# Kernel optimization log

Measured on AMD Instinct MI355X. Metric: run time of the kernel, lower is better.

## Reference

```python
import jax, jax.numpy as jnp
import numpy as np

B, S, H = 2, 2048, 2048
NH, NKV, HD = 16, 4, 128
GROUPS = NH // NKV
THETA = 10000.0
EPS = 1e-6


def setup_inputs() -> dict:
    key = jax.random.key(0)
    ks = jax.random.split(key, 6)
    scale = 0.02
    return {
        "hidden_states": jax.random.normal(ks[0], (B, S, H), jnp.float32),
        "wq": jax.random.normal(ks[1], (NH * HD, H), jnp.float32) * scale,
        "wk": jax.random.normal(ks[2], (NKV * HD, H), jnp.float32) * scale,
        "wv": jax.random.normal(ks[3], (NKV * HD, H), jnp.float32) * scale,
        "wo": jax.random.normal(ks[4], (H, NH * HD), jnp.float32) * scale,
        "q_norm_weight": jnp.ones((HD,), jnp.float32),
        "k_norm_weight": jnp.ones((HD,), jnp.float32),
    }


def _rope_tables(seq_len):
    inv_freq = 1.0 / (THETA ** (jnp.arange(0, HD, 2, dtype=jnp.float32) / HD))
    t = jnp.arange(seq_len, dtype=jnp.float32)
    freqs = jnp.outer(t, inv_freq)              # [S, HD/2]
    emb = jnp.concatenate([freqs, freqs], -1)   # [S, HD]
    return jnp.cos(emb), jnp.sin(emb)


def _rotate_half(x):
    x1, x2 = x[..., : HD // 2], x[..., HD // 2:]
    return jnp.concatenate([-x2, x1], -1)


def _rmsnorm(x, w):
    var = jnp.mean(jnp.square(x), axis=-1, keepdims=True)
    return x * jax.lax.rsqrt(var + EPS) * w


def reference(hidden_states, wq, wk, wv, wo, q_norm_weight, k_norm_weight):
    b, s, _ = hidden_states.shape
    q = (hidden_states @ wq.T).reshape(b, s, NH, HD).transpose(0, 2, 1, 3)    # [b,nh,s,d]
    k = (hidden_states @ wk.T).reshape(b, s, NKV, HD).transpose(0, 2, 1, 3)   # [b,nkv,s,d]
    v = (hidden_states @ wv.T).reshape(b, s, NKV, HD).transpose(0, 2, 1, 3)

    cos, sin = _rope_tables(s)                  # [s,d]
    q = q * cos + _rotate_half(q) * sin
    k = k * cos + _rotate_half(k) * sin

    # fused QK RMSNorm (applied inside fused_qknorm_flash_attention)
    q = _rmsnorm(q, q_norm_weight)
    k = _rmsnorm(k, k_norm_weight)

    # GQA: share each kv head across GROUPS query heads without materializing repeats
    qg = q.reshape(b, NKV, GROUPS, s, HD)
    scale = 1.0 / jnp.sqrt(jnp.float32(HD))
    scores = jnp.einsum('bhgqd,bhkd->bhgqk', qg, k) * scale   # [b,nkv,g,s,s]
    causal = jnp.tril(jnp.ones((s, s), bool))
    scores = jnp.where(causal, scores, jnp.finfo(scores.dtype).min)
    probs = jax.nn.softmax(scores, axis=-1)
    out = jnp.einsum('bhgqk,bhkd->bhgqd', probs, v)            # [b,nkv,g,s,d]
    out = out.reshape(b, NH, s, HD).transpose(0, 2, 1, 3).reshape(b, s, NH * HD)
    return out @ wo.T
```

## Files before the change

kernel.cpp:

```cpp
#include <hip/hip_runtime.h>
#include <math.h>

typedef __bf16 bf16;
typedef __bf16 bf16x8 __attribute__((ext_vector_type(8)));
typedef __bf16 bf16x4 __attribute__((ext_vector_type(4)));
typedef float f32x4 __attribute__((ext_vector_type(4)));

#define B_DIM 2
#define S_LEN 2048
#define H_DIM 2048
#define NH 16
#define NKV 4
#define HD 128

__device__ __forceinline__ void gl_lds16(const void* g, void* l) {
    __builtin_amdgcn_global_load_lds(
        (const __attribute__((address_space(1))) unsigned int*)g,
        (__attribute__((address_space(3))) unsigned int*)l, 16, 0, 0);
}

__device__ __forceinline__ void bar() {
    asm volatile("" ::: "memory");
    __builtin_amdgcn_s_barrier();
    asm volatile("" ::: "memory");
}

__global__ __launch_bounds__(256) void cast_all(const float* __restrict__ s0,
                                                const float* __restrict__ s1,
                                                const float* __restrict__ s2,
                                                const float* __restrict__ s3,
                                                const float* __restrict__ s4,
                                                bf16* __restrict__ dst) {
    const int i = blockIdx.x * 256 + threadIdx.x;
    const float* src;
    int off;
    if (i < 2097152)      { src = s0; off = 0; }
    else if (i < 3145728) { src = s1; off = 2097152; }
    else if (i < 3407872) { src = s2; off = 3145728; }
    else if (i < 3670016) { src = s3; off = 3407872; }
    else                  { src = s4; off = 3670016; }
    float4 f = ((const float4*)src)[i - off];
    bf16x4 o = { (bf16)f.x, (bf16)f.y, (bf16)f.z, (bf16)f.w };
    *(bf16x4*)(dst + (size_t)i * 4) = o;
}

template <typename OutT>
__global__ __launch_bounds__(512, 2) void gemm256(const bf16* __restrict__ A,
                                                  const bf16* __restrict__ Bt,
                                                  OutT* __restrict__ C,
                                                  int M, int N, int K) {
    __shared__ __align__(16) bf16 smem[65536];
    const int t = threadIdx.x, lane = t & 63, w = t >> 6;
    const int lr = lane & 15, quad = lane >> 4;
    const int nN = N >> 8;
    const int nwg = gridDim.x, chunk = nwg >> 3;
    const int bid = blockIdx.x;
    const int lid = (bid & 7) * chunk + (bid >> 3);
    const int m0 = (lid / nN) << 8, n0 = (lid % nN) << 8;
    const int mh_w = w >> 2;
    const int wn = (w & 3) << 6;
    const int nh_w = (w & 3) >> 1;
    const int rb = (w & 1) << 6;
    const int nK = K >> 6;
    const int nIter = K >> 7;

    const int ld0 = w * 2;
    const int lrow = lane >> 2;
    const int csrc = (lane & 3) ^ ((lane >> 3) & 3);
    const int swz = (lr >> 1) & 3;

    auto stA = [&](int ts, int mh) {
        if (ts < nK) {
            bf16* db = smem + (ts & 1) * 16384 + mh * 8192;
            const bf16* sp = A + (size_t)(m0 + mh * 128) * K + ts * 64;
#pragma unroll
            for (int i = 0; i < 2; i++) {
                const int ldi = ld0 + i, kb = ldi >> 3, rg = ldi & 7;
                gl_lds16(sp + (size_t)(rg * 16 + lrow) * K + kb * 32 + csrc * 8,
                         db + kb * 4096 + rg * 512);
            }
        }
    };
    auto stB = [&](int ts, int nh) {
        if (ts < nK) {
            bf16* db = smem + 32768 + (ts & 1) * 16384 + nh * 8192;
            const bf16* sp = Bt + (size_t)(n0 + nh * 128) * K + ts * 64;
#pragma unroll
            for (int i = 0; i < 2; i++) {
                const int ldi = ld0 + i, kb = ldi >> 3, rg = ldi & 7;
                gl_lds16(sp + (size_t)(rg * 16 + lrow) * K + kb * 32 + csrc * 8,
                         db + kb * 4096 + rg * 512);
            }
        }
    };

    f32x4 acc[8][4];
#pragma unroll
    for (int i = 0; i < 8; i++)
#pragma unroll
        for (int j = 0; j < 4; j++) acc[i][j] = (f32x4){0.f, 0.f, 0.f, 0.f};
    bf16x8 af[8], b0[4], b1[4];

    auto rdA = [&](int s, int fi0) {
        const bf16* bp = smem + s * 16384 + mh_w * 8192;
#pragma unroll
        for (int f = 0; f < 4; f++)
#pragma unroll
            for (int ks = 0; ks < 2; ks++)
                af[f * 2 + ks] = *(const bf16x8*)(bp + ks * 4096 +
                                                  ((fi0 + f) * 16 + lr) * 32 + (quad ^ swz) * 8);
    };
    auto rdB = [&](int s, int fj0, bf16x8* dst) {
        const bf16* bp = smem + 32768 + s * 16384 + nh_w * 8192;
#pragma unroll
        for (int f = 0; f < 2; f++)
#pragma unroll
            for (int ks = 0; ks < 2; ks++)
                dst[f * 2 + ks] = *(const bf16x8*)(bp + ks * 4096 +
                                                   (rb + (fj0 + f) * 16 + lr) * 32 + (quad ^ swz) * 8);
    };
    auto mm16 = [&](int fi0, int fj0, bf16x8* bb) {
        __builtin_amdgcn_s_setprio(1);
#pragma unroll
        for (int f = 0; f < 4; f++)
#pragma unroll
            for (int g = 0; g < 2; g++)
#pragma unroll
                for (int ks = 0; ks < 2; ks++)
                    acc[fi0 + f][fj0 + g] = __builtin_amdgcn_mfma_f32_16x16x32_bf16(
                        af[f * 2 + ks], bb[g * 2 + ks], acc[fi0 + f][fj0 + g], 0, 0, 0);
        __builtin_amdgcn_s_setprio(0);
    };

    stA(0, 0); stA(0, 1); stB(0, 0); stB(0, 1); stA(1, 0);
    asm volatile("s_waitcnt vmcnt(2)" ::: "memory");
    bar();

    for (int i = 0; i < nIter; i++) {
        const int ts0 = 2 * i;
#pragma unroll
        for (int h = 0; h < 2; h++) {
            const int ts = ts0 + h, s = h;
            rdA(s, 0); rdB(s, 0, b0);
            stA(ts + 1, 1);
            bar();
            mm16(0, 0, b0);
            bar();
            rdB(s, 2, b1);
            stB(ts + 1, 0);
            bar();
            mm16(0, 2, b1);
            bar();
            rdA(s, 4);
            stB(ts + 1, 1);
            bar();
            mm16(4, 2, b1);
            bar();
            rdB(s, 0, b0);
            stA(ts + 2, 0);
            bar();
            mm16(4, 0, b0);
            if (ts + 2 < nK) asm volatile("s_waitcnt vmcnt(2)" ::: "memory");
            else             asm volatile("s_waitcnt vmcnt(0)" ::: "memory");
            bar();
        }
    }
#pragma unroll
    for (int fi = 0; fi < 8; fi++) {
        const int m = m0 + mh_w * 128 + fi * 16 + quad * 4;
#pragma unroll
        for (int fj = 0; fj < 4; fj++) {
            const int n = n0 + wn + fj * 16 + lr;
#pragma unroll
            for (int r = 0; r < 4; r++)
                C[(size_t)(m + r) * N + n] = (OutT)acc[fi][fj][r];
        }
    }
}

__global__ __launch_bounds__(256) void rope_rms(const bf16* __restrict__ qkv,
                                                const float* __restrict__ qw,
                                                const float* __restrict__ kw,
                                                bf16* __restrict__ qb,
                                                bf16* __restrict__ kb,
                                                bf16* __restrict__ vt) {
    const int tok = blockIdx.x;
    const int b = tok >> 11, s = tok & (S_LEN - 1);
    const int lane = threadIdx.x & 63, w = threadIdx.x >> 6;
    const bf16* row = qkv + (size_t)tok * 3072;
    const float inv = expf(-(float)lane * (9.210340371976184f / 64.f));
    const float ang = (float)s * inv;
    float s_, c_;
    sincosf(ang, &s_, &c_);
    const float wq1 = qw[lane], wq2 = qw[lane + 64];
    const float wk1 = kw[lane], wk2 = kw[lane + 64];
    for (int u = w; u < 24; u += 4) {
        if (u < 16) {
            const float x1 = (float)row[u * 128 + lane], x2 = (float)row[u * 128 + 64 + lane];
            float y1 = x1 * c_ - x2 * s_;
            float y2 = x2 * c_ + x1 * s_;
            float ss = y1 * y1 + y2 * y2;
#pragma unroll
            for (int m = 1; m < 64; m <<= 1) ss += __shfl_xor(ss, m);
            const float r = rsqrtf(ss * (1.f / 128.f) + 1e-6f);
            size_t o = ((size_t)(b * NH + u) * S_LEN + s) * HD;
            qb[o + lane]      = (bf16)(y1 * r * wq1);
            qb[o + 64 + lane] = (bf16)(y2 * r * wq2);
        } else if (u < 20) {
            const int kh = u - 16;
            const float x1 = (float)row[2048 + kh * 128 + lane], x2 = (float)row[2048 + kh * 128 + 64 + lane];
            float y1 = x1 * c_ - x2 * s_;
            float y2 = x2 * c_ + x1 * s_;
            float ss = y1 * y1 + y2 * y2;
#pragma unroll
            for (int m = 1; m < 64; m <<= 1) ss += __shfl_xor(ss, m);
            const float r = rsqrtf(ss * (1.f / 128.f) + 1e-6f);
            size_t base = (size_t)(b * NKV + kh) * 16 * 16384;
            kb[base + (size_t)(lane >> 3) * 16384 + s * 8 + (lane & 7)]       = (bf16)(y1 * r * wk1);
            kb[base + (size_t)(8 + (lane >> 3)) * 16384 + s * 8 + (lane & 7)] = (bf16)(y2 * r * wk2);
        } else {
            const int vh = u - 20;
            const float x1 = (float)row[2560 + vh * 128 + lane], x2 = (float)row[2560 + vh * 128 + 64 + lane];
            const int m = s & 31;
            const int gi = (s >> 5) * 4 + ((m & 15) >> 2);
            const int el = ((m >> 4) << 2) | (m & 3);
            size_t base = ((size_t)(b * NKV + vh) * 256 + gi) * 1024 + el;
            vt[base + (size_t)lane * 8]        = (bf16)x1;
            vt[base + (size_t)(lane + 64) * 8] = (bf16)x2;
        }
    }
}

__global__ __launch_bounds__(256, 3) void flash(const bf16* __restrict__ qg,
                                                const bf16* __restrict__ kg,
                                                const bf16* __restrict__ vg,
                                                bf16* __restrict__ attn,
                                                float* __restrict__ part_o,
                                                float* __restrict__ part_l) {
    static const unsigned char QT[22] = {9,8,15,15,7,14,14,13,13,6,12,12,11,11,5,10,10,4,3,2,1,0};
    static const unsigned char CK[22] = {2,2,0,1,2,0,1,0,1,2,0,1,0,1,2,0,1,2,2,2,2,2};
    const int idx = blockIdx.x;
    const int g = idx >> 5, hb = idx & 31;
    const int qt = QT[g], ck = CK[g];
    const int h = hb & 15, b = hb >> 4;
    const int kvh = h >> 2;
    const int ktBeg = (ck == 1) ? (qt + 1) : 0;
    const int ktEnd = (ck == 0) ? (qt + 1) : (2 * qt + 2);
    const bf16* qh = qg + (size_t)(b * NH + h) * S_LEN * HD;
    const bf16* kh = kg + (size_t)(b * NKV + kvh) * (16 * 16384);
    const bf16* vh = vg + (size_t)(b * NKV + kvh) * (256 * 1024);
    __shared__ __align__(16) bf16 Ks[2][16 * 512];
    __shared__ __align__(16) bf16 Vs[8 * 1024];
    const int t = threadIdx.x, lane = t & 63, w = t >> 6, lr = lane & 15, quad = lane >> 4;
    const int row0 = qt * 128 + w * 32;
    bf16x8 qf[2][4];
#pragma unroll
    for (int mg = 0; mg < 2; mg++)
#pragma unroll
        for (int c = 0; c < 4; c++)
            qf[mg][c] = *(const bf16x8*)(qh + (size_t)(row0 + mg * 16 + lr) * HD + c * 32 + quad * 8);
    f32x4 o[2][8];
    f32x4 lacc[2];
#pragma unroll
    for (int mg = 0; mg < 2; mg++) {
        lacc[mg] = (f32x4){0.f, 0.f, 0.f, 0.f};
#pragma unroll
        for (int j = 0; j < 8; j++) o[mg][j] = (f32x4){0.f, 0.f, 0.f, 0.f};
    }
    const bf16 one = (bf16)1.0f;
    const bf16x8 ones8 = {one, one, one, one, one, one, one, one};
    const float C1 = 0.12751744f;
    const float C2 = -17.3123405f;

    auto stageK = [&](int kt_) {
        if (kt_ < ktEnd) {
            bf16* dst = Ks[kt_ & 1];
            const int kb = kt_ * 64;
#pragma unroll
            for (int i = 0; i < 4; i++) {
                const int dc = w * 4 + i;
                gl_lds16(kh + (size_t)dc * 16384 + (size_t)kb * 8 + lane * 8, dst + dc * 512);
            }
        }
    };
    auto stageV = [&](int kt_) {
#pragma unroll
        for (int i = 0; i < 2; i++) {
            const int c = w * 2 + i;
            const bf16* src = vh + (size_t)(8 * kt_ + c) * 1024 + lane * 8;
            gl_lds16(src, &Vs[c * 1024]);
            gl_lds16(src + 512, &Vs[c * 1024 + 512]);
        }
    };

    stageK(ktBeg);
    stageK(ktBeg + 1);
    __syncthreads();

    for (int kt = ktBeg; kt < ktEnd; ++kt) {
        const int kbase = kt * 64;
        const int cur = kt & 1;
        stageV(kt);
        f32x4 sacc[2][4];
#pragma unroll
        for (int mg = 0; mg < 2; mg++)
#pragma unroll
            for (int n = 0; n < 4; n++) sacc[mg][n] = (f32x4){0.f, 0.f, 0.f, 0.f};
#pragma unroll
        for (int n = 0; n < 4; n++)
#pragma unroll
            for (int c = 0; c < 4; c++) {
                bf16x8 kf = *(const bf16x8*)&Ks[cur][(c * 4 + quad) * 512 + (n * 16 + lr) * 8];
                sacc[0][n] = __builtin_amdgcn_mfma_f32_16x16x32_bf16(kf, qf[0][c], sacc[0][n], 0, 0, 0);
                sacc[1][n] = __builtin_amdgcn_mfma_f32_16x16x32_bf16(kf, qf[1][c], sacc[1][n], 0, 0, 0);
            }
        const bool diag = (kt >= 2 * qt);
        bf16x8 pT[2][2];
#pragma unroll
        for (int mg = 0; mg < 2; mg++) {
            const int qrow = row0 + mg * 16 + lr;
#pragma unroll
            for (int n = 0; n < 4; n++)
#pragma unroll
                for (int r = 0; r < 4; r++) {
                    float ev = exp2f(fmaf(sacc[mg][n][r], C1, C2));
                    if (diag) {
                        const int key = kbase + n * 16 + quad * 4 + r;
                        ev = (key <= qrow) ? ev : 0.f;
                    }
                    pT[mg][n >> 1][(n & 1) * 4 + r] = (bf16)ev;
                }
        }
        asm volatile("s_waitcnt vmcnt(0)" ::: "memory");
        bar();
        stageK(kt + 2);
#pragma unroll
        for (int k2 = 0; k2 < 2; k2++) {
#pragma unroll
            for (int j = 0; j < 8; j++) {
                bf16x8 vf = *(const bf16x8*)&Vs[(k2 * 4 + quad) * 1024 + (j * 16 + lr) * 8];
                o[0][j] = __builtin_amdgcn_mfma_f32_16x16x32_bf16(vf, pT[0][k2], o[0][j], 0, 0, 0);
                o[1][j] = __builtin_amdgcn_mfma_f32_16x16x32_bf16(vf, pT[1][k2], o[1][j], 0, 0, 0);
            }
            lacc[0] = __builtin_amdgcn_mfma_f32_16x16x32_bf16(ones8, pT[0][k2], lacc[0], 0, 0, 0);
            lacc[1] = __builtin_amdgcn_mfma_f32_16x16x32_bf16(ones8, pT[1][k2], lacc[1], 0, 0, 0);
        }
        bar();
    }
    if (ck == 2) {
#pragma unroll
        for (int mg = 0; mg < 2; mg++) {
            const float inv = 1.0f / lacc[mg][0];
            const int qrow = row0 + mg * 16 + lr;
            bf16* dst = attn + ((size_t)(b * S_LEN) + qrow) * (NH * HD) + h * HD + quad * 4;
#pragma unroll
            for (int j = 0; j < 8; j++) {
                bf16x4 st = { (bf16)(o[mg][j][0] * inv), (bf16)(o[mg][j][1] * inv),
                              (bf16)(o[mg][j][2] * inv), (bf16)(o[mg][j][3] * inv) };
                *(bf16x4*)(dst + j * 16) = st;
            }
        }
    } else {
        const int slot = ((b * NH + h) * 6 + (qt - 10)) * 2 + ck;
        float* po = part_o + (size_t)slot * 16384;
#pragma unroll
        for (int mg = 0; mg < 2; mg++) {
            const int row = w * 32 + mg * 16 + lr;
#pragma unroll
            for (int j = 0; j < 8; j++) {
                float4 st = { o[mg][j][0], o[mg][j][1], o[mg][j][2], o[mg][j][3] };
                *(float4*)(po + row * 128 + j * 16 + quad * 4) = st;
            }
            if (quad == 0) part_l[slot * 128 + row] = lacc[mg][0];
        }
    }
}

__global__ __launch_bounds__(256) void reduce_attn(const float* __restrict__ part_o,
                                                   const float* __restrict__ part_l,
                                                   bf16* __restrict__ attn) {
    const int blk = blockIdx.x;
    const int qt = (blk % 6) + 10;
    const int h = (blk / 6) & 15, b = blk / 96;
    const float* p0 = part_o + (size_t)(blk * 2 + 0) * 16384;
    const float* p1 = part_o + (size_t)(blk * 2 + 1) * 16384;
    const float* l0 = part_l + (blk * 2 + 0) * 128;
    const float* l1 = part_l + (blk * 2 + 1) * 128;
    const int t = threadIdx.x;
#pragma unroll
    for (int it = 0; it < 16; it++) {
        const int idx = it * 256 + t;
        const int row = idx >> 5, d4 = idx & 31;
        float4 a = ((const float4*)p0)[idx];
        float4 c = ((const float4*)p1)[idx];
        const float inv = 1.0f / (l0[row] + l1[row]);
        bf16x4 ov = { (bf16)((a.x + c.x) * inv), (bf16)((a.y + c.y) * inv),
                      (bf16)((a.z + c.z) * inv), (bf16)((a.w + c.w) * inv) };
        *(bf16x4*)(attn + ((size_t)(b * S_LEN) + qt * 128 + row) * (NH * HD) + h * HD + d4 * 4) = ov;
    }
}

extern "C" void kernel_launch(void* const* d_in, const int* in_sizes, int n_in,
                              void* d_out, int out_size, void* d_ws, size_t ws_size,
                              hipStream_t stream) {
    (void)in_sizes; (void)n_in; (void)out_size; (void)ws_size;
    const float* hs  = (const float*)d_in[0];
    const float* wq  = (const float*)d_in[1];
    const float* wk  = (const float*)d_in[2];
    const float* wv  = (const float*)d_in[3];
    const float* wo  = (const float*)d_in[4];
    const float* qnw = (const float*)d_in[5];
    const float* knw = (const float*)d_in[6];
    float* out = (float*)d_out;

    char* ws = (char*)d_ws;
    size_t off = 0;
    auto alloc = [&](size_t bytes) {
        void* p = ws + off;
        off += (bytes + 255) & ~(size_t)255;
        return p;
    };
    bf16* hs_bf   = (bf16*)alloc((size_t)4096 * 2048 * 2);
    bf16* wqkv_bf = (bf16*)alloc((size_t)3072 * 2048 * 2);
    bf16* wo_bf   = (bf16*)alloc((size_t)2048 * 2048 * 2);
    bf16* qkv_bf  = (bf16*)alloc((size_t)4096 * 3072 * 2);
    bf16* q_bf    = (bf16*)alloc((size_t)B_DIM * NH * S_LEN * HD * 2);
    bf16* k_bf    = (bf16*)alloc((size_t)B_DIM * NKV * S_LEN * HD * 2);
    bf16* vt_bf   = (bf16*)alloc((size_t)B_DIM * NKV * S_LEN * HD * 2);
    bf16* at_bf   = (bf16*)alloc((size_t)4096 * 2048 * 2);

    float* part_o = (float*)hs_bf;
    float* part_l = (float*)((char*)hs_bf + (size_t)384 * 16384 * 4);

    cast_all<<<18432, 256, 0, stream>>>(hs, wq, wk, wv, wo, hs_bf);
    gemm256<bf16><<<dim3(192), 512, 0, stream>>>(hs_bf, wqkv_bf, qkv_bf, 4096, 3072, 2048);
    rope_rms<<<4096, 256, 0, stream>>>(qkv_bf, qnw, knw, q_bf, k_bf, vt_bf);
    flash<<<dim3(704), 256, 0, stream>>>(q_bf, k_bf, vt_bf, at_bf, part_o, part_l);
    reduce_attn<<<dim3(192), 256, 0, stream>>>(part_o, part_l, at_bf);
    gemm256<float><<<dim3(128), 512, 0, stream>>>(at_bf, wo_bf, out, 4096, 2048, 2048);
}
```

Measured before the change: 313.2 us.

## Use 256x128 tile GEMM for output projection to fill more CUs

Adds a gemm_pn kernel that uses 256x128 output tiles, so the output projection launches 256 workgroups instead of 128 and covers more of the device's compute units. It also turns the main GEMM's two-step unrolled K loop into a single per-tile loop, and reorders the QK MFMA loop in flash attention so the K dimension is the outer loop. The new kernel waits for all outstanding loads (vmcnt(0)) on every iteration, which limits how much load latency it can overlap, and smaller tiles cost more operand traffic per output element.

```diff
diff --git a/kernel.cpp b/kernel.cpp
--- a/kernel.cpp
+++ b/kernel.cpp
@@ -62,7 +62,6 @@
     const int nh_w = (w & 3) >> 1;
     const int rb = (w & 1) << 6;
     const int nK = K >> 6;
-    const int nIter = K >> 7;
 
     const int ld0 = w * 2;
     const int lrow = lane >> 2;
@@ -136,34 +135,30 @@
     asm volatile("s_waitcnt vmcnt(2)" ::: "memory");
     bar();
 
-    for (int i = 0; i < nIter; i++) {
-        const int ts0 = 2 * i;
-#pragma unroll
-        for (int h = 0; h < 2; h++) {
-            const int ts = ts0 + h, s = h;
-            rdA(s, 0); rdB(s, 0, b0);
-            stA(ts + 1, 1);
-            bar();
-            mm16(0, 0, b0);
-            bar();
-            rdB(s, 2, b1);
-            stB(ts + 1, 0);
-            bar();
-            mm16(0, 2, b1);
-            bar();
-            rdA(s, 4);
-            stB(ts + 1, 1);
-            bar();
-            mm16(4, 2, b1);
-            bar();
-            rdB(s, 0, b0);
-            stA(ts + 2, 0);
-            bar();
-            mm16(4, 0, b0);
-            if (ts + 2 < nK) asm volatile("s_waitcnt vmcnt(2)" ::: "memory");
-            else             asm volatile("s_waitcnt vmcnt(0)" ::: "memory");
-            bar();
-        }
+    for (int ts = 0; ts < nK; ++ts) {
+        const int s = ts & 1;
+        rdA(s, 0); rdB(s, 0, b0);
+        stA(ts + 1, 1);
+        bar();
+        mm16(0, 0, b0);
+        bar();
+        rdB(s, 2, b1);
+        stB(ts + 1, 0);
+        bar();
+        mm16(0, 2, b1);
+        bar();
+        rdA(s, 4);
+        stB(ts + 1, 1);
+        bar();
+        mm16(4, 2, b1);
+        bar();
+        rdB(s, 0, b0);
+        stA(ts + 2, 0);
+        bar();
+        mm16(4, 0, b0);
+        if (ts + 2 < nK) asm volatile("s_waitcnt vmcnt(2)" ::: "memory");
+        else             asm volatile("s_waitcnt vmcnt(0)" ::: "memory");
+        bar();
     }
 #pragma unroll
     for (int fi = 0; fi < 8; fi++) {
@@ -174,6 +169,125 @@
 #pragma unroll
             for (int r = 0; r < 4; r++)
                 C[(size_t)(m + r) * N + n] = (OutT)acc[fi][fj][r];
+        }
+    }
+}
+
+__global__ __launch_bounds__(512, 1) void gemm_pn(const bf16* __restrict__ A,
+                                                  const bf16* __restrict__ Bt,
+                                                  float* __restrict__ C,
+                                                  int M, int N, int K) {
+    __shared__ __align__(16) bf16 smem[49152];
+    const int t = threadIdx.x, lane = t & 63, w = t >> 6;
+    const int lr = lane & 15, quad = lane >> 4;
+    const int nN = N >> 7;
+    const int nwg = gridDim.x, chunk = nwg >> 3;
+    const int bid = blockIdx.x;
+    const int lid = (bid & 7) * chunk + (bid >> 3);
+    const int m0 = (lid / nN) << 8, n0 = (lid % nN) << 7;
+    const int mh_w = w >> 2;
+    const int wn = (w & 3) << 5;
+    const int nK = K >> 6;
+
+    const int ld0 = w * 2;
+    const int lrow = lane >> 2;
+    const int csrc = (lane & 3) ^ ((lane >> 3) & 3);
+    const int swz = (lr >> 1) & 3;
+
+    auto stA = [&](int ts, int mh) {
+        if (ts < nK) {
+            bf16* db = smem + (ts & 1) * 16384 + mh * 8192;
+            const bf16* sp = A + (size_t)(m0 + mh * 128) * K + ts * 64;
+#pragma unroll
+            for (int i = 0; i < 2; i++) {
+                const int ldi = ld0 + i, kb = ldi >> 3, rg = ldi & 7;
+                gl_lds16(sp + (size_t)(rg * 16 + lrow) * K + kb * 32 + csrc * 8,
+                         db + kb * 4096 + rg * 512);
+            }
+        }
+    };
+    auto stB1 = [&](int ts) {
+        if (ts < nK) {
+            bf16* db = smem + 32768 + (ts & 1) * 8192;
+            const bf16* sp = Bt + (size_t)n0 * K + ts * 64;
+#pragma unroll
+            for (int i = 0; i < 2; i++) {
+                const int ldi = ld0 + i, kb = ldi >> 3, rg = ldi & 7;
+                gl_lds16(sp + (size_t)(rg * 16 + lrow) * K + kb * 32 + csrc * 8,
+                         db + kb * 4096 + rg * 512);
+            }
+        }
+    };
+
+    f32x4 acc[8][2];
+#pragma unroll
+    for (int i = 0; i < 8; i++)
+#pragma unroll
+        for (int j = 0; j < 2; j++) acc[i][j] = (f32x4){0.f, 0.f, 0.f, 0.f};
+    bf16x8 af[8], bf1[4];
+
+    auto rdA = [&](int s, int fi0) {
+        const bf16* bp = smem + s * 16384 + mh_w * 8192;
+#pragma unroll
+        for (int f = 0; f < 4; f++)
+#pragma unroll
+            for (int ks = 0; ks < 2; ks++)
+                af[f * 2 + ks] = *(const bf16x8*)(bp + ks * 4096 +
+                                                  ((fi0 + f) * 16 + lr) * 32 + (quad ^ swz) * 8);
+    };
+    auto rdB1 = [&](int s) {
+        const bf16* bp = smem + 32768 + s * 8192;
+#pragma unroll
+        for (int f = 0; f < 2; f++)
+#pragma unroll
+            for (int ks = 0; ks < 2; ks++)
+                bf1[f * 2 + ks] = *(const bf16x8*)(bp + ks * 4096 +
+                                                   (wn + f * 16 + lr) * 32 + (quad ^ swz) * 8);
+    };
+    auto mm8 = [&](int fi0, int ks) {
+        __builtin_amdgcn_s_setprio(1);
+#pragma unroll
+        for (int f = 0; f < 4; f++)
+#pragma unroll
+            for (int g = 0; g < 2; g++)
+                acc[fi0 + f][g] = __builtin_amdgcn_mfma_f32_16x16x32_bf16(
+                    af[f * 2 + ks], bf1[g * 2 + ks], acc[fi0 + f][g], 0, 0, 0);
+        __builtin_amdgcn_s_setprio(0);
+    };
+
+    stA(0, 0); stA(0, 1); stB1(0);
+    asm volatile("s_waitcnt vmcnt(0)" ::: "memory");
+    bar();
+
+    for (int ts = 0; ts < nK; ++ts) {
+        const int s = ts & 1;
+        rdA(s, 0); rdB1(s);
+        stA(ts + 1, 0);
+        bar();
+        mm8(0, 0);
+        bar();
+        stA(ts + 1, 1);
+        stB1(ts + 1);
+        bar();
+        mm8(0, 1);
+        bar();
+        rdA(s, 4);
+        bar();
+        mm8(4, 0);
+        bar();
+        mm8(4, 1);
+        asm volatile("s_waitcnt vmcnt(0)" ::: "memory");
+        bar();
+    }
+#pragma unroll
+    for (int fi = 0; fi < 8; fi++) {
+        const int m = m0 + mh_w * 128 + fi * 16 + quad * 4;
+#pragma unroll
+        for (int fj = 0; fj < 2; fj++) {
+            const int n = n0 + wn + fj * 16 + lr;
+#pragma unroll
+            for (int r = 0; r < 4; r++)
+                C[(size_t)(m + r) * N + n] = acc[fi][fj][r];
         }
     }
 }
@@ -307,9 +421,9 @@
 #pragma unroll
             for (int n = 0; n < 4; n++) sacc[mg][n] = (f32x4){0.f, 0.f, 0.f, 0.f};
 #pragma unroll
-        for (int n = 0; n < 4; n++)
-#pragma unroll
-            for (int c = 0; c < 4; c++) {
+        for (int c = 0; c < 4; c++)
+#pragma unroll
+            for (int n = 0; n < 4; n++) {
                 bf16x8 kf = *(const bf16x8*)&Ks[cur][(c * 4 + quad) * 512 + (n * 16 + lr) * 8];
                 sacc[0][n] = __builtin_amdgcn_mfma_f32_16x16x32_bf16(kf, qf[0][c], sacc[0][n], 0, 0, 0);
                 sacc[1][n] = __builtin_amdgcn_mfma_f32_16x16x32_bf16(kf, qf[1][c], sacc[1][n], 0, 0, 0);
@@ -437,5 +551,5 @@
     rope_rms<<<4096, 256, 0, stream>>>(qkv_bf, qnw, knw, q_bf, k_bf, vt_bf);
     flash<<<dim3(704), 256, 0, stream>>>(q_bf, k_bf, vt_bf, at_bf, part_o, part_l);
     reduce_attn<<<dim3(192), 256, 0, stream>>>(part_o, part_l, at_bf);
-    gemm256<float><<<dim3(128), 512, 0, stream>>>(at_bf, wo_bf, out, 4096, 2048, 2048);
-}
+    gemm_pn<<<dim3(256), 512, 0, stream>>>(at_bf, wo_bf, out, 4096, 2048, 2048);
+}
```

New measurement: 307.6 us. No clear change (-1.8%).
